# Kernel tuning notes

Measured on AMD Instinct MI355X. Metric: run time of the kernel, lower is better.

## Reference

```python
import jax, jax.numpy as jnp
import numpy as np

BQ = 64  # query block size
BK = 64  # key block size
PV_SCALE = 1e-3  # pvthreshd (~0..50) -> prob threshold, mirrors int8 P-quantization cutoff


def setup_inputs() -> dict:
    key = jax.random.key(0)
    ks = jax.random.split(key, 6)
    B, H, L, D = 2, 16, 2048, 64
    q = jax.random.normal(ks[0], (B, H, L, D), jnp.float32)
    k = jax.random.normal(ks[1], (B, H, L, D), jnp.float32)
    v = jax.random.normal(ks[2], (B, H, L, D), jnp.float32)
    # per-head tuned thresholds (init defaults / autotune ranges)
    cdfthreshd = 0.85 + 0.14 * jax.random.uniform(ks[3], (H,), jnp.float32)
    simthreshd1 = jax.random.uniform(ks[4], (H,), jnp.float32, minval=-0.3, maxval=0.5)
    pvthreshd = jax.random.uniform(ks[5], (H,), jnp.float32, minval=15.0, maxval=25.0)
    return dict(q=q, k=k, v=v, cdfthreshd=cdfthreshd,
                simthreshd1=simthreshd1, pvthreshd=pvthreshd)


def _sparse_meansim_attention(q, k, v, cdfthreshd, simthreshd1, pvthreshd):
    B, H, L, D = q.shape
    nqb, nkb = L // BQ, L // BK
    scale = 1.0 / jnp.sqrt(jnp.float32(D))

    # smooth_k: subtract per-(B,H) key mean along sequence
    k = k - k.mean(axis=2, keepdims=True)

    qb = q.reshape(B, H, nqb, BQ, D)
    kb = k.reshape(B, H, nkb, BK, D)
    qm = qb.mean(axis=3)  # [B,H,nqb,D]
    km = kb.mean(axis=3)  # [B,H,nkb,D]

    # mean cosine similarity of queries to their block mean -> pooled (prunable) blocks
    qn = jnp.linalg.norm(qb, axis=-1)            # [B,H,nqb,BQ]
    qmn = jnp.linalg.norm(qm, axis=-1)           # [B,H,nqb]
    cos = jnp.einsum('bhnqd,bhnd->bhnq', qb, qm) / (qn * qmn[..., None] + 1e-6)
    pooled = cos.mean(axis=-1) > simthreshd1[None, :, None]  # [B,H,nqb]

    # block-level score map from pooled means, CDF-based top-mass block selection
    s = jnp.einsum('bhid,bhjd->bhij', qm, km) * scale        # [B,H,nqb,nkb]
    p = jax.nn.softmax(s, axis=-1)
    order = jnp.argsort(-p, axis=-1)
    p_sorted = jnp.take_along_axis(p, order, axis=-1)
    excl_cdf = jnp.cumsum(p_sorted, axis=-1) - p_sorted      # exclusive CDF
    keep_sorted = excl_cdf < cdfthreshd[None, :, None, None]
    keep = jnp.take_along_axis(keep_sorted, jnp.argsort(order, axis=-1), axis=-1)

    sink = (jnp.arange(nkb) == 0)  # attention_sink: always keep first key block
    block_mask = keep | (~pooled)[..., None] | sink          # [B,H,nqb,nkb]

    # full attention restricted to selected blocks
    S = jnp.einsum('bhqd,bhkd->bhqk', q, k) * scale          # [B,H,L,L]
    m = jnp.repeat(jnp.repeat(block_mask, BQ, axis=2), BK, axis=3)
    P = jax.nn.softmax(jnp.where(m, S, -jnp.inf), axis=-1)

    # second-stage PV pruning: skip PV accumulation for negligible prob blocks
    Pb = P.reshape(B, H, nqb, BQ, nkb, BK)
    pv_keep = Pb.max(axis=(3, 5)) >= pvthreshd[None, :, None, None] * PV_SCALE
    pv_keep = pv_keep | sink
    Pb = Pb * pv_keep[:, :, :, None, :, None].astype(P.dtype)

    o = jnp.einsum('bhqk,bhkd->bhqd', Pb.reshape(B, H, L, L), v)
    return o


def reference(q, k, v, cdfthreshd, simthreshd1, pvthreshd):
    return _sparse_meansim_attention(q, k, v, cdfthreshd, simthreshd1, pvthreshd)
```

## Files before the change

kernel.cpp:

```cpp
#include <hip/hip_runtime.h>
#include <hip/hip_bf16.h>
#include <math.h>
#include <stdint.h>

#define B 2
#define H 16
#define L 2048
#define D 64
#define NB 32
#define PTS 72

typedef unsigned short u16;
typedef unsigned int u32;
typedef __attribute__((ext_vector_type(2))) unsigned int u32x2;
typedef __attribute__((ext_vector_type(8))) short s16x8;
typedef __attribute__((ext_vector_type(4))) float f32x4;

union FragU { s16x8 v; u32 u[4]; };

__device__ __forceinline__ u32 pkbf(float a, float b) {
  __hip_bfloat162 h = __float22bfloat162_rn(make_float2(a, b));
  union { __hip_bfloat162 h; u32 u; } cv; cv.h = h; return cv.u;
}
__device__ __forceinline__ float bf2f(u32 u16bits) {
  union { u32 u; float f; } c; c.u = u16bits << 16; return c.f;
}
__device__ __forceinline__ void split4(float4 p, u32x2& hi, u32x2& lo) {
  u32 h01 = pkbf(p.x, p.y), h23 = pkbf(p.z, p.w);
  float rx = p.x - bf2f(h01 & 0xffffu);
  float ry = p.y - bf2f(h01 >> 16);
  float rz = p.z - bf2f(h23 & 0xffffu);
  float rw = p.w - bf2f(h23 >> 16);
  hi = (u32x2){h01, h23};
  lo = (u32x2){pkbf(rx, ry), pkbf(rz, rw)};
}

__global__ __launch_bounds__(256) void k_prep(const float* __restrict__ k,
                                              const float* __restrict__ v,
                                              float* __restrict__ ksum,
                                              u16* __restrict__ khi_g,
                                              u16* __restrict__ klo_g,
                                              u16* __restrict__ vthi_g,
                                              u16* __restrict__ vtlo_g,
                                              float* __restrict__ kbmax) {
  int blk = blockIdx.x, bh = blk >> 5, j = blk & 31, t = threadIdx.x;
  __shared__ float vt[64 * 65];
  __shared__ float pk_[4][64];
  __shared__ unsigned bmaxS;
  if (t == 0) bmaxS = 0u;
  size_t base = (size_t)blk * 4096;
  {
    int d = t & 63, g = t >> 6;
    float sk = 0.f;
    for (int r = g * 16; r < g * 16 + 16; ++r) sk += k[base + r * 64 + d];
    pk_[g][d] = sk;
  }
  __syncthreads();
  if (t < 64) ksum[(size_t)blk * 64 + t] = pk_[0][t] + pk_[1][t] + pk_[2][t] + pk_[3][t];

  float rmax = 0.f;
  for (int it = 0; it < 4; ++it) {
    int idx = t + 256 * it, r = idx >> 4, c4 = (idx & 15) * 4;
    float4 f = *(const float4*)(k + base + r * 64 + c4);
    u32x2 hi, lo; split4(f, hi, lo);
    *(u32x2*)(khi_g + base + r * 64 + c4) = hi;
    *(u32x2*)(klo_g + base + r * 64 + c4) = lo;
    float ssq = f.x*f.x + f.y*f.y + f.z*f.z + f.w*f.w;
    ssq += __shfl_xor(ssq, 1); ssq += __shfl_xor(ssq, 2);
    ssq += __shfl_xor(ssq, 4); ssq += __shfl_xor(ssq, 8);
    if ((t & 15) == 0) rmax = fmaxf(rmax, ssq);
    float4 g2 = *(const float4*)(v + base + r * 64 + c4);
    vt[(c4 + 0) * 65 + r] = g2.x;
    vt[(c4 + 1) * 65 + r] = g2.y;
    vt[(c4 + 2) * 65 + r] = g2.z;
    vt[(c4 + 3) * 65 + r] = g2.w;
  }
  if ((t & 15) == 0) atomicMax(&bmaxS, __float_as_uint(rmax));
  __syncthreads();
  if (t == 0) kbmax[blk] = __uint_as_float(bmaxS);
  for (int it = 0; it < 2; ++it) {
    int idx = t + 256 * it, d = idx >> 3, s8 = (idx & 7) * 8;
    const float* vr = &vt[d * 65 + s8];
    float4 f0 = {vr[0], vr[1], vr[2], vr[3]};
    float4 f1 = {vr[4], vr[5], vr[6], vr[7]};
    u32x2 h0, l0, h1, l1;
    split4(f0, h0, l0); split4(f1, h1, l1);
    size_t o = (size_t)bh * 131072 + (size_t)d * 2048 + j * 64 + s8;
    *(u32x2*)(vthi_g + o) = h0; *(u32x2*)(vthi_g + o + 4) = h1;
    *(u32x2*)(vtlo_g + o) = l0; *(u32x2*)(vtlo_g + o + 4) = l1;
  }
}

#define RBM_OFF 36864
#define MS_OFF 53760
#define LINV_OFF 54272
#define LPART_OFF 54784
#define QM_OFF 56832
#define FLG_OFF 57344

__global__ __launch_bounds__(256, 2) void k_attn(
    const float* __restrict__ q,
    const float* __restrict__ ksum,
    const u16* __restrict__ khi_g, const u16* __restrict__ klo_g,
    const u16* __restrict__ vthi_g, const u16* __restrict__ vtlo_g,
    const float* __restrict__ cdfthreshd, const float* __restrict__ simthreshd1,
    const float* __restrict__ pvthreshd, const float* __restrict__ kbmax,
    float* __restrict__ out) {
  int blk = blockIdx.x, bh = blk >> 4, ip = blk & 15, h = bh & (H - 1);
  int t = threadIdx.x, lane = t & 63, w = t >> 6;
  int m16 = lane & 15, quad = lane >> 4;

  __shared__ __align__(16) uint8_t smem[57376];
  u16*   pbase = (u16*)smem;
  u32*   rbm0  = (u32*)(smem + RBM_OFF);
  float* MS    = (float*)(smem + MS_OFF);
  float* linvS = (float*)(smem + LINV_OFF);
  float* lpart = (float*)(smem + LPART_OFF);
  float* qmS   = (float*)(smem + QM_OFF);
  int*   flg   = (int*)(smem + FLG_OFF);
#define PHQ(qb) (pbase + (qb) * 9216)
#define PLQ(qb) (pbase + 4608 + (qb) * 9216)

  const float* qg0 = q + ((size_t)bh * L + (size_t)(2 * ip) * 64) * D;
  const float* qg1 = qg0 + 64 * D;
  const u16* kh = khi_g + (size_t)bh * (L * D);
  const u16* kl = klo_g + (size_t)bh * (L * D);
  const u16* vh = vthi_g + (size_t)bh * (L * D);
  const u16* vl = vtlo_g + (size_t)bh * (L * D);

  s16x8 qhf[2][4][2], qlf[2][4][2];
#pragma unroll
  for (int qb = 0; qb < 2; ++qb) {
    const float* qgq = qb ? qg1 : qg0;
#pragma unroll
    for (int nt = 0; nt < 4; ++nt)
#pragma unroll
      for (int ks = 0; ks < 2; ++ks) {
        const float* p0 = qgq + (16 * nt + m16) * 64 + ks * 32 + quad * 8;
        float4 a = *(const float4*)p0;
        float4 b2 = *(const float4*)(p0 + 4);
        u32x2 ha, la, hb, lb;
        split4(a, ha, la); split4(b2, hb, lb);
        FragU fh, fl;
        fh.u[0] = ha[0]; fh.u[1] = ha[1]; fh.u[2] = hb[0]; fh.u[3] = hb[1];
        fl.u[0] = la[0]; fl.u[1] = la[1]; fl.u[2] = lb[0]; fl.u[3] = lb[1];
        qhf[qb][nt][ks] = fh.v; qlf[qb][nt][ks] = fl.v;
      }
  }
  for (int e = t; e < 2 * 64 * 33; e += 256)
    rbm0[e] = 0x7F800000u;

  if (w == 0 || w == 2) {
    int qb = w >> 1;
    const float* qgq = qb ? qg1 : qg0;
    float s = 0.f;
    for (int r = 0; r < 64; ++r) s += qgq[r * 64 + lane];
    qmS[qb * 64 + lane] = s * (1.f / 64.f);
  }
  if (w == 1) {
    float m = (lane < 32) ? kbmax[bh * 32 + lane] : 0.f;
    for (int off = 16; off; off >>= 1) m = fmaxf(m, __shfl_xor(m, off, 32));
    if (lane == 0) ((float*)flg)[6] = m;
  }
  __syncthreads();

  bool keepj = false;
  if ((w == 0 || w == 2) && lane < 32) {
    int qb = w >> 1, j = lane;
    const float* qmv = qmS + qb * 64;
    const float* ksp = ksum + (size_t)bh * NB * 64 + j * 64;
    float sv = 0.f;
    for (int d = 0; d < 64; ++d) sv += qmv[d] * ksp[d];
    sv *= (1.f / 64.f) * 0.125f;
    float mx = sv;
    for (int off = 16; off; off >>= 1) mx = fmaxf(mx, __shfl_xor(mx, off, 32));
    float p = expf(sv - mx);
    float sum = p;
    for (int off = 16; off; off >>= 1) sum += __shfl_xor(sum, off, 32);
    p /= sum;
    float excl = 0.f;
    for (int u = 0; u < 32; ++u) {
      float pu = __shfl(p, u, 32);
      if ((pu > p) || (pu == p && u < j)) excl += pu;
    }
    keepj = excl < cdfthreshd[h];
  }
  if (w == 1 || w == 3) {
    int qb = w >> 1, r = lane;
    const float* qgq = qb ? qg1 : qg0;
    const float* qmv = qmS + qb * 64;
    float kmax2 = ((float*)flg)[6];
    float dot = 0.f, qn2 = 0.f, qmn2 = 0.f;
    for (int d = 0; d < 64; ++d) {
      float a = qgq[r * 64 + d], b2 = qmv[d];
      dot += a * b2; qn2 += a * a; qmn2 += b2 * b2;
    }
    float cs = dot / (sqrtf(qn2) * sqrtf(qmn2) + 1e-6f);
    float su = cs;
    for (int off = 32; off; off >>= 1) su += __shfl_xor(su, off);
    if (lane == 0) flg[qb] = (su * (1.f / 64.f)) > simthreshd1[h];
    MS[qb * 64 + r] = sqrtf(qn2 * kmax2) * 0.125f;
  }
  __syncthreads();
  if ((w == 0 || w == 2) && lane < 32) {
    int qb = w >> 1;
    bool bit = keepj || !flg[qb] || (lane == 0);
    unsigned long long bal = __ballot(bit);
    if (lane == 0) flg[2 + qb] = (int)(u32)bal;
  }
  __syncthreads();
  u32 mw0 = (u32)flg[2], mw1 = (u32)flg[3];

  float Mq[2][4];
#pragma unroll
  for (int qb = 0; qb < 2; ++qb)
#pragma unroll
    for (int nt = 0; nt < 4; ++nt) Mq[qb][nt] = MS[qb * 64 + 16 * nt + m16];

  float lp[2][4] = {{0.f,0.f,0.f,0.f},{0.f,0.f,0.f,0.f}};
  {
    u32 mwU = mw0 | mw1;
    int j = (int)__builtin_ctz(mwU);
    u32 rm_ = mwU & (mwU - 1);
    s16x8 ka[2][2], kan[2][2];
    {
      const u16* kr0 = kh + (size_t)(j * 64 + 16 * w + m16) * 64 + quad * 8;
      const u16* kl0 = kl + (size_t)(j * 64 + 16 * w + m16) * 64 + quad * 8;
#pragma unroll
      for (int ks = 0; ks < 2; ++ks) {
        ka[ks][0] = *(const s16x8*)(kr0 + ks * 32);
        ka[ks][1] = *(const s16x8*)(kl0 + ks * 32);
      }
    }
    for (;;) {
      int nj = -1;
      if (rm_) {
        nj = (int)__builtin_ctz(rm_); rm_ &= rm_ - 1;
        const u16* nr = kh + (size_t)(nj * 64 + 16 * w + m16) * 64 + quad * 8;
        const u16* nl = kl + (size_t)(nj * 64 + 16 * w + m16) * 64 + quad * 8;
#pragma unroll
        for (int ks = 0; ks < 2; ++ks) {
          kan[ks][0] = *(const s16x8*)(nr + ks * 32);
          kan[ks][1] = *(const s16x8*)(nl + ks * 32);
        }
      }
#pragma unroll
      for (int qb = 0; qb < 2; ++qb) {
        u32 mm = qb ? mw1 : mw0;
        if (!((mm >> j) & 1u)) continue;
        f32x4 acc[4];
#pragma unroll
        for (int nt = 0; nt < 4; ++nt) acc[nt] = (f32x4){0.f, 0.f, 0.f, 0.f};
#pragma unroll
        for (int ks = 0; ks < 2; ++ks)
#pragma unroll
          for (int nt = 0; nt < 4; ++nt) {
            acc[nt] = __builtin_amdgcn_mfma_f32_16x16x32_bf16(ka[ks][0], qhf[qb][nt][ks], acc[nt], 0, 0, 0);
            acc[nt] = __builtin_amdgcn_mfma_f32_16x16x32_bf16(ka[ks][1], qhf[qb][nt][ks], acc[nt], 0, 0, 0);
            acc[nt] = __builtin_amdgcn_mfma_f32_16x16x32_bf16(ka[ks][0], qlf[qb][nt][ks], acc[nt], 0, 0, 0);
          }
#pragma unroll
        for (int nt = 0; nt < 4; ++nt) {
          float vmax = -1e30f;
#pragma unroll
          for (int reg = 0; reg < 4; ++reg) {
            float s = acc[nt][reg] * 0.125f - Mq[qb][nt];
            lp[qb][nt] += __expf(s);
            vmax = fmaxf(vmax, s);
          }
          vmax = fmaxf(vmax, __shfl_xor(vmax, 16));
          vmax = fmaxf(vmax, __shfl_xor(vmax, 32));
          if (quad == 0)
            atomicMin(rbm0 + qb * (64 * 33) + (16 * nt + m16) * 33 + j,
                      __float_as_uint(fmaxf(-vmax, 0.f)));
        }
      }
      if (nj < 0) break;
#pragma unroll
      for (int ks = 0; ks < 2; ++ks) { ka[ks][0] = kan[ks][0]; ka[ks][1] = kan[ks][1]; }
      j = nj;
    }
  }
#pragma unroll
  for (int qb = 0; qb < 2; ++qb)
#pragma unroll
    for (int nt = 0; nt < 4; ++nt) {
      float s = lp[qb][nt];
      s += __shfl_xor(s, 16); s += __shfl_xor(s, 32);
      if (quad == 0) lpart[w * 128 + qb * 64 + 16 * nt + m16] = s;
    }
  __syncthreads();
  if (t < 128) linvS[t] = 1.f / (lpart[t] + lpart[128 + t] + lpart[256 + t] + lpart[384 + t]);
  __syncthreads();

  if (w < 2 && lane < 32) {
    u32 mm = w ? mw1 : mw0;
    bool keep = (mm >> lane) & 1u;
    if (keep && lane != 0) {
      float thr = pvthreshd[h] * 1e-3f;
      const float* lin = linvS + w * 64;
      const u32* rb = rbm0 + w * (64 * 33);
      float mp = 0.f;
      for (int r = 0; r < 64; ++r) {
        float key = __uint_as_float(rb[r * 33 + lane]);
        mp = fmaxf(mp, __expf(-key) * lin[r]);
      }
      keep = mp >= thr;
    }
    unsigned long long bal = __ballot(keep);
    if (lane == 0) flg[4 + w] = (int)(u32)bal;
  }
  __syncthreads();
  u32 gm0 = (u32)flg[4], gm1 = (u32)flg[5];

  float linq[2][4];
#pragma unroll
  for (int qb = 0; qb < 2; ++qb)
#pragma unroll
    for (int nt = 0; nt < 4; ++nt) linq[qb][nt] = linvS[qb * 64 + 16 * nt + m16];
  f32x4 oacc[2][4];
#pragma unroll
  for (int qb = 0; qb < 2; ++qb)
#pragma unroll
    for (int nt = 0; nt < 4; ++nt) oacc[qb][nt] = (f32x4){0.f, 0.f, 0.f, 0.f};

  {
    u32 gmU = gm0 | gm1;
    int j = -1;
    u32 g2 = gmU;
    s16x8 ka[2][2];
    if (g2) {
      j = (int)__builtin_ctz(g2); g2 &= g2 - 1;
      const u16* kr0 = kh + (size_t)(j * 64 + 16 * w + m16) * 64 + quad * 8;
      const u16* kl0 = kl + (size_t)(j * 64 + 16 * w + m16) * 64 + quad * 8;
#pragma unroll
      for (int ks = 0; ks < 2; ++ks) {
        ka[ks][0] = *(const s16x8*)(kr0 + ks * 32);
        ka[ks][1] = *(const s16x8*)(kl0 + ks * 32);
      }
    }
    while (j >= 0) {
      int in0 = (gm0 >> j) & 1, in1 = (gm1 >> j) & 1;
      s16x8 va[2][2];
      {
        const u16* vr0 = vh + (size_t)(16 * w + m16) * L + j * 64 + quad * 8;
        const u16* vl0 = vl + (size_t)(16 * w + m16) * L + j * 64 + quad * 8;
#pragma unroll
        for (int ks = 0; ks < 2; ++ks) {
          va[ks][0] = *(const s16x8*)(vr0 + ks * 32);
          va[ks][1] = *(const s16x8*)(vl0 + ks * 32);
        }
      }
      f32x4 acc[4];
      if (in0) {
#pragma unroll
        for (int nt = 0; nt < 4; ++nt) acc[nt] = (f32x4){0.f, 0.f, 0.f, 0.f};
#pragma unroll
        for (int ks = 0; ks < 2; ++ks)
#pragma unroll
          for (int nt = 0; nt < 4; ++nt) {
            acc[nt] = __builtin_amdgcn_mfma_f32_16x16x32_bf16(ka[ks][0], qhf[0][nt][ks], acc[nt], 0, 0, 0);
            acc[nt] = __builtin_amdgcn_mfma_f32_16x16x32_bf16(ka[ks][1], qhf[0][nt][ks], acc[nt], 0, 0, 0);
            acc[nt] = __builtin_amdgcn_mfma_f32_16x16x32_bf16(ka[ks][0], qlf[0][nt][ks], acc[nt], 0, 0, 0);
          }
      }
      __syncthreads();
      if (in0) {
#pragma unroll
        for (int nt = 0; nt < 4; ++nt) {
          float4 pv;
          pv.x = __expf(acc[nt][0] * 0.125f - Mq[0][nt]) * linq[0][nt];
          pv.y = __expf(acc[nt][1] * 0.125f - Mq[0][nt]) * linq[0][nt];
          pv.z = __expf(acc[nt][2] * 0.125f - Mq[0][nt]) * linq[0][nt];
          pv.w = __expf(acc[nt][3] * 0.125f - Mq[0][nt]) * linq[0][nt];
          u32x2 hi, lo; split4(pv, hi, lo);
          int off = (16 * nt + m16) * PTS + 16 * w + 4 * quad;
          *(u32x2*)(PHQ(0) + off) = hi;
          *(u32x2*)(PLQ(0) + off) = lo;
        }
      }
      if (in1) {
#pragma unroll
        for (int nt = 0; nt < 4; ++nt) acc[nt] = (f32x4){0.f, 0.f, 0.f, 0.f};
#pragma unroll
        for (int ks = 0; ks < 2; ++ks)
#pragma unroll
          for (int nt = 0; nt < 4; ++nt) {
            acc[nt] = __builtin_amdgcn_mfma_f32_16x16x32_bf16(ka[ks][0], qhf[1][nt][ks], acc[nt], 0, 0, 0);
            acc[nt] = __builtin_amdgcn_mfma_f32_16x16x32_bf16(ka[ks][1], qhf[1][nt][ks], acc[nt], 0, 0, 0);
            acc[nt] = __builtin_amdgcn_mfma_f32_16x16x32_bf16(ka[ks][0], qlf[1][nt][ks], acc[nt], 0, 0, 0);
          }
#pragma unroll
        for (int nt = 0; nt < 4; ++nt) {
          float4 pv;
          pv.x = __expf(acc[nt][0] * 0.125f - Mq[1][nt]) * linq[1][nt];
          pv.y = __expf(acc[nt][1] * 0.125f - Mq[1][nt]) * linq[1][nt];
          pv.z = __expf(acc[nt][2] * 0.125f - Mq[1][nt]) * linq[1][nt];
          pv.w = __expf(acc[nt][3] * 0.125f - Mq[1][nt]) * linq[1][nt];
          u32x2 hi, lo; split4(pv, hi, lo);
          int off = (16 * nt + m16) * PTS + 16 * w + 4 * quad;
          *(u32x2*)(PHQ(1) + off) = hi;
          *(u32x2*)(PLQ(1) + off) = lo;
        }
      }
      int nj = -1;
      if (g2) {
        nj = (int)__builtin_ctz(g2); g2 &= g2 - 1;
        const u16* nr = kh + (size_t)(nj * 64 + 16 * w + m16) * 64 + quad * 8;
        const u16* nl = kl + (size_t)(nj * 64 + 16 * w + m16) * 64 + quad * 8;
#pragma unroll
        for (int ks = 0; ks < 2; ++ks) {
          ka[ks][0] = *(const s16x8*)(nr + ks * 32);
          ka[ks][1] = *(const s16x8*)(nl + ks * 32);
        }
      }
      __syncthreads();
#pragma unroll
      for (int qb = 0; qb < 2; ++qb) {
        if (!(qb ? in1 : in0)) continue;
        const u16* ph_ = PHQ(qb);
        const u16* pl_ = PLQ(qb);
#pragma unroll
        for (int ks = 0; ks < 2; ++ks)
#pragma unroll
          for (int nt = 0; nt < 4; ++nt) {
            s16x8 pbh = *(const s16x8*)(ph_ + (16 * nt + m16) * PTS + ks * 32 + quad * 8);
            s16x8 pbl = *(const s16x8*)(pl_ + (16 * nt + m16) * PTS + ks * 32 + quad * 8);
            oacc[qb][nt] = __builtin_amdgcn_mfma_f32_16x16x32_bf16(va[ks][0], pbh, oacc[qb][nt], 0, 0, 0);
            oacc[qb][nt] = __builtin_amdgcn_mfma_f32_16x16x32_bf16(va[ks][1], pbh, oacc[qb][nt], 0, 0, 0);
            oacc[qb][nt] = __builtin_amdgcn_mfma_f32_16x16x32_bf16(va[ks][0], pbl, oacc[qb][nt], 0, 0, 0);
          }
      }
      j = nj;
    }
  }

#pragma unroll
  for (int qb = 0; qb < 2; ++qb) {
    float* ob = out + ((size_t)bh * L + (size_t)(2 * ip + qb) * 64) * D;
#pragma unroll
    for (int nt = 0; nt < 4; ++nt)
      *(f32x4*)(ob + (16 * nt + m16) * 64 + 16 * w + 4 * quad) = oacc[qb][nt];
  }
}

extern "C" void kernel_launch(void* const* d_in, const int* in_sizes, int n_in,
                              void* d_out, int out_size, void* d_ws, size_t ws_size,
                              hipStream_t stream) {
  (void)in_sizes; (void)n_in; (void)out_size; (void)ws_size;
  const float* q   = (const float*)d_in[0];
  const float* k   = (const float*)d_in[1];
  const float* v   = (const float*)d_in[2];
  const float* cdf = (const float*)d_in[3];
  const float* sim = (const float*)d_in[4];
  const float* pvt = (const float*)d_in[5];
  float* out = (float*)d_out;

  uint8_t* w8 = (uint8_t*)d_ws;
  float* ksum  = (float*)w8;
  float* kbmax = (float*)(w8 + 262144);
  u16* khi_g  = (u16*)(w8 + 266240);
  u16* klo_g  = khi_g + (size_t)B * H * L * D;
  u16* vthi_g = klo_g + (size_t)B * H * L * D;
  u16* vtlo_g = vthi_g + (size_t)B * H * L * D;

  k_prep<<<B * H * NB, 256, 0, stream>>>(k, v, ksum, khi_g, klo_g, vthi_g, vtlo_g, kbmax);
  k_attn<<<B * H * NB / 2, 256, 0, stream>>>(q, ksum, khi_g, klo_g, vthi_g, vtlo_g,
                                             cdf, sim, pvt, kbmax, out);
}
```

Baseline: 224.5 us.

## Restructure key prep into single pass and remap attention block order

The prep kernel now reads each K/V row once with 8-wide vector loads. It computes column sums through shuffle reductions instead of a separate strided pass, and the bf16 hi/lo stores widen to 128-bit. This is meant to cut redundant global reads and the number of store instructions. Separately, the attention kernel remaps blockIdx so that consecutive workgroups are spread across head/batch groups, likely to balance load or L2 locality across XCDs. The remap changes the scheduling pattern, and its effect on cache reuse is uncertain.

```diff
diff --git a/kernel.cpp b/kernel.cpp
--- a/kernel.cpp
+++ b/kernel.cpp
@@ -13,6 +13,7 @@
 typedef unsigned short u16;
 typedef unsigned int u32;
 typedef __attribute__((ext_vector_type(2))) unsigned int u32x2;
+typedef __attribute__((ext_vector_type(4))) unsigned int u32x4;
 typedef __attribute__((ext_vector_type(8))) short s16x8;
 typedef __attribute__((ext_vector_type(4))) float f32x4;
 
@@ -44,40 +45,60 @@
                                               u16* __restrict__ vtlo_g,
                                               float* __restrict__ kbmax) {
   int blk = blockIdx.x, bh = blk >> 5, j = blk & 31, t = threadIdx.x;
+  int lane = t & 63, w = t >> 6;
   __shared__ float vt[64 * 65];
   __shared__ float pk_[4][64];
   __shared__ unsigned bmaxS;
   if (t == 0) bmaxS = 0u;
   size_t base = (size_t)blk * 4096;
-  {
-    int d = t & 63, g = t >> 6;
-    float sk = 0.f;
-    for (int r = g * 16; r < g * 16 + 16; ++r) sk += k[base + r * 64 + d];
-    pk_[g][d] = sk;
+
+  int r0 = t >> 3;
+  int c8 = (t & 7) * 8;
+  float cs[8] = {0.f, 0.f, 0.f, 0.f, 0.f, 0.f, 0.f, 0.f};
+  float rmax = 0.f;
+#pragma unroll
+  for (int it = 0; it < 2; ++it) {
+    int r = r0 + 32 * it;
+    const float* kp = k + base + r * 64 + c8;
+    float4 f0 = *(const float4*)kp;
+    float4 f1 = *(const float4*)(kp + 4);
+    u32x2 h0, l0, h1, l1;
+    split4(f0, h0, l0); split4(f1, h1, l1);
+    *(u32x4*)(khi_g + base + r * 64 + c8) = (u32x4){h0[0], h0[1], h1[0], h1[1]};
+    *(u32x4*)(klo_g + base + r * 64 + c8) = (u32x4){l0[0], l0[1], l1[0], l1[1]};
+    cs[0] += f0.x; cs[1] += f0.y; cs[2] += f0.z; cs[3] += f0.w;
+    cs[4] += f1.x; cs[5] += f1.y; cs[6] += f1.z; cs[7] += f1.w;
+    float ssq = f0.x*f0.x + f0.y*f0.y + f0.z*f0.z + f0.w*f0.w
+              + f1.x*f1.x + f1.y*f1.y + f1.z*f1.z + f1.w*f1.w;
+    ssq += __shfl_xor(ssq, 1); ssq += __shfl_xor(ssq, 2); ssq += __shfl_xor(ssq, 4);
+    if ((t & 7) == 0) rmax = fmaxf(rmax, ssq);
+    const float* vp = v + base + r * 64 + c8;
+    float4 g0 = *(const float4*)vp;
+    float4 g1 = *(const float4*)(vp + 4);
+    vt[(c8 + 0) * 65 + r] = g0.x;
+    vt[(c8 + 1) * 65 + r] = g0.y;
+    vt[(c8 + 2) * 65 + r] = g0.z;
+    vt[(c8 + 3) * 65 + r] = g0.w;
+    vt[(c8 + 4) * 65 + r] = g1.x;
+    vt[(c8 + 5) * 65 + r] = g1.y;
+    vt[(c8 + 6) * 65 + r] = g1.z;
+    vt[(c8 + 7) * 65 + r] = g1.w;
+  }
+  if ((t & 7) == 0) atomicMax(&bmaxS, __float_as_uint(rmax));
+#pragma unroll
+  for (int i = 0; i < 8; ++i) {
+    cs[i] += __shfl_xor(cs[i], 8);
+    cs[i] += __shfl_xor(cs[i], 16);
+    cs[i] += __shfl_xor(cs[i], 32);
+  }
+  if (lane < 8) {
+    *(float4*)&pk_[w][lane * 8]     = (float4){cs[0], cs[1], cs[2], cs[3]};
+    *(float4*)&pk_[w][lane * 8 + 4] = (float4){cs[4], cs[5], cs[6], cs[7]};
   }
   __syncthreads();
   if (t < 64) ksum[(size_t)blk * 64 + t] = pk_[0][t] + pk_[1][t] + pk_[2][t] + pk_[3][t];
-
-  float rmax = 0.f;
-  for (int it = 0; it < 4; ++it) {
-    int idx = t + 256 * it, r = idx >> 4, c4 = (idx & 15) * 4;
-    float4 f = *(const float4*)(k + base + r * 64 + c4);
-    u32x2 hi, lo; split4(f, hi, lo);
-    *(u32x2*)(khi_g + base + r * 64 + c4) = hi;
-    *(u32x2*)(klo_g + base + r * 64 + c4) = lo;
-    float ssq = f.x*f.x + f.y*f.y + f.z*f.z + f.w*f.w;
-    ssq += __shfl_xor(ssq, 1); ssq += __shfl_xor(ssq, 2);
-    ssq += __shfl_xor(ssq, 4); ssq += __shfl_xor(ssq, 8);
-    if ((t & 15) == 0) rmax = fmaxf(rmax, ssq);
-    float4 g2 = *(const float4*)(v + base + r * 64 + c4);
-    vt[(c4 + 0) * 65 + r] = g2.x;
-    vt[(c4 + 1) * 65 + r] = g2.y;
-    vt[(c4 + 2) * 65 + r] = g2.z;
-    vt[(c4 + 3) * 65 + r] = g2.w;
-  }
-  if ((t & 15) == 0) atomicMax(&bmaxS, __float_as_uint(rmax));
-  __syncthreads();
   if (t == 0) kbmax[blk] = __uint_as_float(bmaxS);
+#pragma unroll
   for (int it = 0; it < 2; ++it) {
     int idx = t + 256 * it, d = idx >> 3, s8 = (idx & 7) * 8;
     const float* vr = &vt[d * 65 + s8];
@@ -86,8 +107,8 @@
     u32x2 h0, l0, h1, l1;
     split4(f0, h0, l0); split4(f1, h1, l1);
     size_t o = (size_t)bh * 131072 + (size_t)d * 2048 + j * 64 + s8;
-    *(u32x2*)(vthi_g + o) = h0; *(u32x2*)(vthi_g + o + 4) = h1;
-    *(u32x2*)(vtlo_g + o) = l0; *(u32x2*)(vtlo_g + o + 4) = l1;
+    *(u32x4*)(vthi_g + o) = (u32x4){h0[0], h0[1], h1[0], h1[1]};
+    *(u32x4*)(vtlo_g + o) = (u32x4){l0[0], l0[1], l1[0], l1[1]};
   }
 }
 
@@ -106,7 +127,9 @@
     const float* __restrict__ cdfthreshd, const float* __restrict__ simthreshd1,
     const float* __restrict__ pvthreshd, const float* __restrict__ kbmax,
     float* __restrict__ out) {
-  int blk = blockIdx.x, bh = blk >> 4, ip = blk & 15, h = bh & (H - 1);
+  int blk0 = blockIdx.x;
+  int blk = (blk0 & 7) * 64 + (blk0 >> 3);
+  int bh = blk >> 4, ip = blk & 15, h = bh & (H - 1);
   int t = threadIdx.x, lane = t & 63, w = t >> 6;
   int m16 = lane & 15, quad = lane >> 4;
 
```

After: 211.9 us. 5.6% less time.
